# Optimization experiments

Measured on AMD Instinct MI355X. Metric: run time of the kernel, lower is better.

Reference implementation:

```python
import jax, jax.numpy as jnp
import numpy as np

L, K, N, W = 4096, 1, 2, 8
T = L * N // K  # 8192 time steps, matches the original Python loop count
SQRT_HALF = 0.7071067811865476  # stddev sqrt(1/2) of the random channel


def setup_inputs() -> dict:
    key = jax.random.key(0)
    k1, k2 = jax.random.split(key)
    B, C = 32, 128
    x = jax.random.normal(k1, (B, T, C), dtype=jnp.float32)
    h = jax.random.normal(k2, (B, T, C), dtype=jnp.float32) * SQRT_HALF
    return {"x": x, "h": h}


def reference(x, h):
    # x, h: (B, T, 2F) -> split last dim into real/imag halves
    F = x.shape[-1] // 2
    xr, xi = x[..., :F], x[..., F:]
    hr, hi = h[..., :F], h[..., F:]
    # complex multiply hc * xc, then concat real/imag back
    isi = jnp.concatenate([hr * xr - hi * xi, hr * xi + hi * xr], axis=-1)
    B, Tt, C = x.shape
    # causal sliding-window sum: y[i] = sum(isi[max(0, i-W):i]) via prefix sums
    c0 = jnp.concatenate(
        [jnp.zeros((B, 1, C), dtype=x.dtype), jnp.cumsum(isi, axis=1)], axis=1
    )  # (B, T+1, C); c0[:, j] = sum of first j steps
    idx = jnp.arange(Tt)
    y_isi = c0[:, idx] - c0[:, jnp.clip(idx - W, 0)]
    return y_isi + x
```

## Files before the change

kernel.cpp:

```cpp
#include <hip/hip_runtime.h>


typedef float f2 __attribute__((ext_vector_type(2)));

constexpr int TLEN   = 8192;
constexpr int CCH    = 128;
constexpr int FHALF  = 64;
constexpr int WWIN   = 8;
constexpr int TC     = 64;
constexpr int NCHUNK = TLEN / TC;
constexpr int NB     = 32;

__global__ __launch_bounds__(256) void isi_window_kernel(
    const float* __restrict__ x, const float* __restrict__ h,
    float* __restrict__ out)
{
    const int wave = threadIdx.x >> 6;
    const int lane = threadIdx.x & 63;
    const int c2   = (lane & 31) * 2;
    const int half = lane >> 5;

    const int gw    = blockIdx.x * 4 + wave;
    const int col   = gw * 2 + half;
    const int b     = col >> 7;
    const int chunk = col & (NCHUNK - 1);
    const int t0    = chunk * TC;

    const size_t base = (size_t)b * TLEN * CCH + c2;
    const float* xb = x + base;
    const float* hb = h + base;
    float*       ob = out + base;

    f2 histr[WWIN], histi[WWIN];
    f2 winr = (f2)(0.f), wini = (f2)(0.f);
#pragma unroll
    for (int j = 0; j < WWIN; ++j) {
        histr[j] = (f2)(0.f);
        histi[j] = (f2)(0.f);
    }

    if (t0 > 0) {
        const int tw = t0 - WWIN;
#pragma unroll
        for (int j = 0; j < WWIN; ++j) {
            const size_t off = (size_t)(tw + j) * CCH;
            const f2 xr = *(const f2*)(xb + off);
            const f2 xi = *(const f2*)(xb + off + FHALF);
            const f2 hr = *(const f2*)(hb + off);
            const f2 hi = *(const f2*)(hb + off + FHALF);
            const f2 ir = hr * xr - hi * xi;
            const f2 ii = hr * xi + hi * xr;
            histr[j] = ir; histi[j] = ii;
            winr += ir; wini += ii;
        }
    }

    for (int tb = t0; tb < t0 + TC; tb += WWIN) {
#pragma unroll
        for (int j = 0; j < WWIN; ++j) {
            const size_t off = (size_t)(tb + j) * CCH;
            const f2 xr = *(const f2*)(xb + off);
            const f2 xi = *(const f2*)(xb + off + FHALF);
            const f2 hr = *(const f2*)(hb + off);
            const f2 hi = *(const f2*)(hb + off + FHALF);

            const f2 o0 = xr + winr;
            const f2 o1 = xi + wini;
            __builtin_nontemporal_store(o0, (f2*)(ob + off));
            __builtin_nontemporal_store(o1, (f2*)(ob + off + FHALF));

            const f2 ir = hr * xr - hi * xi;
            const f2 ii = hr * xi + hi * xr;

            winr += ir - histr[j];
            wini += ii - histi[j];
            histr[j] = ir; histi[j] = ii;
        }
    }
}

extern "C" void kernel_launch(void* const* d_in, const int* in_sizes, int n_in,
                              void* d_out, int out_size, void* d_ws, size_t ws_size,
                              hipStream_t stream) {
    const float* x = (const float*)d_in[0];
    const float* h = (const float*)d_in[1];
    float* out = (float*)d_out;

    const int total_cols  = NB * NCHUNK;
    const int total_waves = total_cols / 2;
    const int blocks      = total_waves / 4;
    isi_window_kernel<<<blocks, 256, 0, stream>>>(x, h, out);
}
```

Baseline: 66.14 us.

## Share chunk-tail ISI window via LDS to avoid redundant halo loads

Each half-wave first computes the ISI of the last window of its time chunk and publishes it to LDS. After a block barrier, the neighbouring chunk in the same block reads it as its initial history instead of reloading x and h for the halo. Only the first chunk in each block still loads the halo from global memory. This cuts redundant global reads of the halo region (about 1/8 extra traffic) at the cost of 32KB of LDS per block, a __syncthreads, and extra registers holding the tail values, which may lower occupancy.

```diff
diff --git a/kernel.cpp b/kernel.cpp
--- a/kernel.cpp
+++ b/kernel.cpp
@@ -10,18 +10,21 @@
 constexpr int TC     = 64;
 constexpr int NCHUNK = TLEN / TC;
 constexpr int NB     = 32;
+constexpr int CPG    = 8;
 
 __global__ __launch_bounds__(256) void isi_window_kernel(
     const float* __restrict__ x, const float* __restrict__ h,
     float* __restrict__ out)
 {
+    __shared__ float lds[CPG][WWIN][CCH];
+
     const int wave = threadIdx.x >> 6;
     const int lane = threadIdx.x & 63;
     const int c2   = (lane & 31) * 2;
     const int half = lane >> 5;
+    const int k    = wave * 2 + half;
 
-    const int gw    = blockIdx.x * 4 + wave;
-    const int col   = gw * 2 + half;
+    const int col   = blockIdx.x * CPG + k;
     const int b     = col >> 7;
     const int chunk = col & (NCHUNK - 1);
     const int t0    = chunk * TC;
@@ -31,19 +34,36 @@
     const float* hb = h + base;
     float*       ob = out + base;
 
+    f2 xtr[WWIN], xti[WWIN], itr[WWIN], iti[WWIN];
+#pragma unroll
+    for (int j = 0; j < WWIN; ++j) {
+        const size_t off = (size_t)(t0 + TC - WWIN + j) * CCH;
+        const f2 xr = *(const f2*)(xb + off);
+        const f2 xi = *(const f2*)(xb + off + FHALF);
+        const f2 hr = *(const f2*)(hb + off);
+        const f2 hi = *(const f2*)(hb + off + FHALF);
+        const f2 ir = hr * xr - hi * xi;
+        const f2 ii = hr * xi + hi * xr;
+        xtr[j] = xr; xti[j] = xi; itr[j] = ir; iti[j] = ii;
+        *(f2*)&lds[k][j][c2]         = ir;
+        *(f2*)&lds[k][j][FHALF + c2] = ii;
+    }
+    __syncthreads();
+
     f2 histr[WWIN], histi[WWIN];
     f2 winr = (f2)(0.f), wini = (f2)(0.f);
-#pragma unroll
-    for (int j = 0; j < WWIN; ++j) {
-        histr[j] = (f2)(0.f);
-        histi[j] = (f2)(0.f);
-    }
-
-    if (t0 > 0) {
-        const int tw = t0 - WWIN;
+    if (k > 0) {
 #pragma unroll
         for (int j = 0; j < WWIN; ++j) {
-            const size_t off = (size_t)(tw + j) * CCH;
+            const f2 ir = *(const f2*)&lds[k - 1][j][c2];
+            const f2 ii = *(const f2*)&lds[k - 1][j][FHALF + c2];
+            histr[j] = ir; histi[j] = ii;
+            winr += ir; wini += ii;
+        }
+    } else if (chunk > 0) {
+#pragma unroll
+        for (int j = 0; j < WWIN; ++j) {
+            const size_t off = (size_t)(t0 - WWIN + j) * CCH;
             const f2 xr = *(const f2*)(xb + off);
             const f2 xi = *(const f2*)(xb + off + FHALF);
             const f2 hr = *(const f2*)(hb + off);
@@ -53,9 +73,15 @@
             histr[j] = ir; histi[j] = ii;
             winr += ir; wini += ii;
         }
+    } else {
+#pragma unroll
+        for (int j = 0; j < WWIN; ++j) {
+            histr[j] = (f2)(0.f);
+            histi[j] = (f2)(0.f);
+        }
     }
 
-    for (int tb = t0; tb < t0 + TC; tb += WWIN) {
+    for (int tb = t0; tb < t0 + TC - WWIN; tb += WWIN) {
 #pragma unroll
         for (int j = 0; j < WWIN; ++j) {
             const size_t off = (size_t)(tb + j) * CCH;
@@ -77,6 +103,17 @@
             histr[j] = ir; histi[j] = ii;
         }
     }
+
+#pragma unroll
+    for (int j = 0; j < WWIN; ++j) {
+        const size_t off = (size_t)(t0 + TC - WWIN + j) * CCH;
+        const f2 o0 = xtr[j] + winr;
+        const f2 o1 = xti[j] + wini;
+        __builtin_nontemporal_store(o0, (f2*)(ob + off));
+        __builtin_nontemporal_store(o1, (f2*)(ob + off + FHALF));
+        winr += itr[j] - histr[j];
+        wini += iti[j] - histi[j];
+    }
 }
 
 extern "C" void kernel_launch(void* const* d_in, const int* in_sizes, int n_in,
@@ -86,8 +123,7 @@
     const float* h = (const float*)d_in[1];
     float* out = (float*)d_out;
 
-    const int total_cols  = NB * NCHUNK;
-    const int total_waves = total_cols / 2;
-    const int blocks      = total_waves / 4;
+    const int total_cols = NB * NCHUNK;
+    const int blocks     = total_cols / CPG;
     isi_window_kernel<<<blocks, 256, 0, stream>>>(x, h, out);
 }
```

Measured after the change: 63.49 us. 1.04x faster.
